# Performance work log

Hardware: AMD Instinct MI355X
Metric: run time of the kernel (lower is better)

Reference implementation:

```python
import jax, jax.numpy as jnp
import numpy as np

B, S, D, H = 2, 2048, 1024, 16
DK = D // H


def setup_inputs() -> dict:
    key = jax.random.key(0)
    ks = jax.random.split(key, 9)
    w_scale = 0.02  # small init for linear weights
    return {
        "query": jax.random.normal(ks[0], (B, S, D), jnp.float32),
        "key": jax.random.normal(ks[1], (B, S, D), jnp.float32),
        "value": jax.random.normal(ks[2], (B, S, D), jnp.float32),
        "mask": jax.random.randint(ks[3], (B, 1, S, S), 0, 2).astype(bool),
        "Wq": jax.random.normal(ks[4], (D, D), jnp.float32) * w_scale,
        "bq": jnp.zeros((D,), jnp.float32),
        "Wk": jax.random.normal(ks[5], (D, D), jnp.float32) * w_scale,
        "bk": jnp.zeros((D,), jnp.float32),
        "Wv": jax.random.normal(ks[6], (D, D), jnp.float32) * w_scale,
        "bv": jnp.zeros((D,), jnp.float32),
        "Wo": jax.random.normal(ks[7], (D, D), jnp.float32) * w_scale,
        "bo": jnp.zeros((D,), jnp.float32),
    }


def _split_heads(x):
    # [B,S,D] -> [B,H,S,DK]
    return x.reshape(B, S, H, DK).transpose(0, 2, 1, 3)


def reference(query, key, value, mask, Wq, bq, Wk, bk, Wv, bv, Wo, bo):
    Q = _split_heads(query @ Wq + bq)
    K = _split_heads(key @ Wk + bk)
    V = _split_heads(value @ Wv + bv)
    scores = jnp.einsum("bhqd,bhkd->bhqk", Q, K) / jnp.sqrt(jnp.float32(DK))
    scores = jnp.where(mask, -jnp.inf, scores)  # masked_fill(mask, -inf)
    attn_w = jax.nn.softmax(scores, axis=-1)
    attn_w = jnp.nan_to_num(attn_w, nan=0.0)  # rows fully masked -> 0
    out = jnp.einsum("bhqk,bhkd->bhqd", attn_w, V)
    out = out.transpose(0, 2, 1, 3).reshape(B, S, D)
    return out @ Wo + bo
```

## Files before the change

kernel.cpp:

```cpp
#include <hip/hip_runtime.h>
#include <hip/hip_bf16.h>
#include <cmath>
#include <cstdint>
#include <cstddef>

#define B_  2
#define S_  2048
#define D_  1024
#define H_  16
#define DK_ 64
#define NEG_BIG (-1e30f)

typedef __attribute__((ext_vector_type(8))) short bf16x8;
typedef __attribute__((ext_vector_type(4))) float f32x4;
typedef __attribute__((ext_vector_type(16))) float f32x16;

static __device__ __forceinline__ unsigned short f2bf(float f) {
  __hip_bfloat16 h = __float2bfloat16(f);
  return *reinterpret_cast<unsigned short*>(&h);
}

static __device__ __forceinline__ unsigned cvtpk(float lo, float hi) {
  unsigned d;
  asm("v_cvt_pk_bf16_f32 %0, %1, %2" : "=v"(d) : "v"(lo), "v"(hi));
  return d;
}
#define SWAP32(a, b) asm("v_permlane32_swap_b32 %0, %1" : "+v"(a), "+v"(b))

__global__ void pack_mask_kernel(const int* __restrict__ mask,
                                 unsigned* __restrict__ bits, int nwords) {
  int i = blockIdx.x * blockDim.x + threadIdx.x;
  if (i >= nwords) return;
  const int* p = mask + (size_t)i * 32;
  unsigned w = 0;
#pragma unroll
  for (int j = 0; j < 32; ++j) w |= (p[j] != 0 ? (1u << j) : 0u);
  bits[i] = w;
}

__global__ void cvt_f32_bf16_kernel(const float* __restrict__ in,
                                    unsigned short* __restrict__ out, int n8) {
  int i = blockIdx.x * blockDim.x + threadIdx.x;
  if (i >= n8) return;
  const float4* p = reinterpret_cast<const float4*>(in) + (size_t)i * 2;
  float4 a = p[0], b = p[1];
  ushort4 o0 = {f2bf(a.x), f2bf(a.y), f2bf(a.z), f2bf(a.w)};
  ushort4 o1 = {f2bf(b.x), f2bf(b.y), f2bf(b.z), f2bf(b.w)};
  ushort4* q = reinterpret_cast<ushort4*>(out) + (size_t)i * 2;
  q[0] = o0;
  q[1] = o1;
}

__global__ __launch_bounds__(256) void transpose_w_kernel(
    const float* __restrict__ W, unsigned short* __restrict__ Wt) {
  __shared__ unsigned short tile[32][33];
  const int r0 = blockIdx.y * 32, c0 = blockIdx.x * 32;
  const int t = threadIdx.x;
  {
    const int r = t >> 3, c4 = (t & 7) * 4;
    float4 v = *reinterpret_cast<const float4*>(&W[(size_t)(r0 + r) * D_ + c0 + c4]);
    tile[c4 + 0][r] = f2bf(v.x);
    tile[c4 + 1][r] = f2bf(v.y);
    tile[c4 + 2][r] = f2bf(v.z);
    tile[c4 + 3][r] = f2bf(v.w);
  }
  __syncthreads();
  {
    const int n = t >> 3, k4 = (t & 7) * 4;
    ushort4 o = {tile[n][k4 + 0], tile[n][k4 + 1], tile[n][k4 + 2], tile[n][k4 + 3]};
    *reinterpret_cast<ushort4*>(&Wt[(size_t)(c0 + n) * D_ + r0 + k4]) = o;
  }
}

template <int MODE>
__global__ __launch_bounds__(256) void gemm_bf16_kernel(
    const unsigned short* __restrict__ A, const unsigned short* __restrict__ Wt,
    const float* __restrict__ bias, void* __restrict__ Cout) {
  constexpr int K = D_;
  __shared__ __attribute__((aligned(16))) unsigned short as_[64 * 32];
  __shared__ __attribute__((aligned(16))) unsigned short bs_[64 * 32];
  const int bm = blockIdx.x * 64, bn = blockIdx.y * 64;
  const int t = threadIdx.x, wv = t >> 6, lane = t & 63;
  const int r = lane & 15, g = lane >> 4;
  const int wm = (wv >> 1) * 32, wn = (wv & 1) * 32;
  const int grow = 16 * wv + (lane >> 2);
  const int gcol = (lane & 3) * 8;

  typedef __attribute__((address_space(3))) unsigned int lds_u32;
  typedef __attribute__((address_space(1))) const unsigned int glb_u32;
  lds_u32* asl = (lds_u32*)(as_ + 16 * wv * 32);
  lds_u32* bsl = (lds_u32*)(bs_ + 16 * wv * 32);

  f32x4 acc[2][2] = {};

  for (int k0 = 0; k0 < K; k0 += 32) {
    __syncthreads();
    __builtin_amdgcn_global_load_lds(
        (glb_u32*)&A[(size_t)(bm + grow) * K + k0 + gcol], asl, 16, 0, 0);
    __builtin_amdgcn_global_load_lds(
        (glb_u32*)&Wt[(size_t)(bn + grow) * K + k0 + gcol], bsl, 16, 0, 0);
    __syncthreads();

    bf16x8 a0 = *reinterpret_cast<const bf16x8*>(&as_[(wm + r) * 32 + 8 * g]);
    bf16x8 a1 = *reinterpret_cast<const bf16x8*>(&as_[(wm + 16 + r) * 32 + 8 * g]);
    bf16x8 b0 = *reinterpret_cast<const bf16x8*>(&bs_[(wn + r) * 32 + 8 * g]);
    bf16x8 b1 = *reinterpret_cast<const bf16x8*>(&bs_[(wn + 16 + r) * 32 + 8 * g]);
    acc[0][0] = __builtin_amdgcn_mfma_f32_16x16x32_bf16(a0, b0, acc[0][0], 0, 0, 0);
    acc[0][1] = __builtin_amdgcn_mfma_f32_16x16x32_bf16(a0, b1, acc[0][1], 0, 0, 0);
    acc[1][0] = __builtin_amdgcn_mfma_f32_16x16x32_bf16(a1, b0, acc[1][0], 0, 0, 0);
    acc[1][1] = __builtin_amdgcn_mfma_f32_16x16x32_bf16(a1, b1, acc[1][1], 0, 0, 0);
  }

#pragma unroll
  for (int mf = 0; mf < 2; ++mf)
#pragma unroll
    for (int nf = 0; nf < 2; ++nf)
#pragma unroll
      for (int reg = 0; reg < 4; ++reg) {
        const int row = bm + wm + 16 * mf + 4 * g + reg;
        const int col = bn + wn + 16 * nf + r;
        float v = acc[mf][nf][reg] + bias[col];
        if constexpr (MODE == 3) {
          ((float*)Cout)[(size_t)row * D_ + col] = v;
        } else {
          const int bb = row >> 11, s = row & (S_ - 1);
          const int h = col >> 6, dk = col & (DK_ - 1);
          unsigned short* o = (unsigned short*)Cout;
          if constexpr (MODE == 0)
            o[(((size_t)(bb * H_ + h)) * S_ + s) * DK_ + dk] = f2bf(v * 0.125f);
          else if constexpr (MODE == 1)
            o[(((size_t)(bb * H_ + h)) * S_ + s) * DK_ + dk] = f2bf(v);
          else
            o[(((size_t)(bb * H_ + h)) * DK_ + dk) * S_ + s] = f2bf(v);
        }
      }
}

__global__ __launch_bounds__(256) void attn_mfma_kernel(
    const unsigned short* __restrict__ Qh, const unsigned short* __restrict__ Kh,
    const unsigned short* __restrict__ VT, const unsigned* __restrict__ mbits,
    unsigned short* __restrict__ ctx) {
  __shared__ float mlds[2][2][32];
  __shared__ float llds[2][2][32];
  __shared__ float olds[2][2][16][64];

  const int flat = blockIdx.x;
  const int bh = (flat & 7) * 4 + ((flat >> 3) & 3);
  const int qblk = flat >> 5;
  const int b = bh >> 4, h = bh & 15;
  const int wv = threadIdx.x >> 6, lane = threadIdx.x & 63;
  const int qsub = wv & 1, khalf = wv >> 1;
  const int ql = lane & 31, hi = lane >> 5;
  const int qrow = qblk * 64 + qsub * 32 + ql;

  const unsigned short* Qrow = &Qh[((size_t)bh * S_ + qrow) * DK_];
  bf16x8 qf[4];
#pragma unroll
  for (int i = 0; i < 4; ++i)
    qf[i] = *(const bf16x8*)&Qrow[16 * i + 8 * hi];

  const unsigned short* Khead = &Kh[(size_t)bh * S_ * DK_];
  const unsigned short* Vhead = &VT[(size_t)bh * DK_ * S_];
  const unsigned* mrow = &mbits[((size_t)b * S_ + qrow) * (S_ / 32)];

  f32x16 o0 = {}, o1 = {};
  float m = NEG_BIG, l = 0.f;

  const int tbeg = khalf * 32, tend = tbeg + 32;
  bf16x8 kf[4];
#pragma unroll
  for (int i = 0; i < 4; ++i)
    kf[i] = *(const bf16x8*)&Khead[(size_t)(tbeg * 32 + ql) * DK_ + 16 * i + 8 * hi];
  unsigned mw = mrow[tbeg];

  for (int tt = tbeg; tt < tend; ++tt) {
    f32x16 sc = {};
#pragma unroll
    for (int i = 0; i < 4; ++i)
      sc = __builtin_amdgcn_mfma_f32_32x32x16_bf16(kf[i], qf[i], sc, 0, 0, 0);

    const int tn = (tt + 1 < tend) ? tt + 1 : tt;
    bf16x8 kn[4];
#pragma unroll
    for (int i = 0; i < 4; ++i)
      kn[i] = *(const bf16x8*)&Khead[(size_t)(tn * 32 + ql) * DK_ + 16 * i + 8 * hi];
    const unsigned mwn = mrow[tn];

    bf16x8 vf[2][2];
#pragma unroll
    for (int kk = 0; kk < 2; ++kk)
#pragma unroll
      for (int db = 0; db < 2; ++db)
        vf[kk][db] = *(const bf16x8*)
            &Vhead[(size_t)(db * 32 + ql) * S_ + tt * 32 + kk * 16 + 8 * hi];

    const unsigned msh = mw >> (4 * hi);
#pragma unroll
    for (int reg = 0; reg < 16; ++reg) {
      const int creg = (reg & 3) + 8 * (reg >> 2);
      if ((msh >> creg) & 1u) sc[reg] = NEG_BIG;
    }

    float px = sc[0];
#pragma unroll
    for (int reg = 1; reg < 16; ++reg) px = fmaxf(px, sc[reg]);
    px = fmaxf(px, __shfl_xor(px, 32));

    if (!__all(px - m <= 8.f)) {
      const float mn = fmaxf(m, px);
      const float alpha = __expf(m - mn);
      m = mn;
      l *= alpha;
#pragma unroll
      for (int reg = 0; reg < 16; ++reg) { o0[reg] *= alpha; o1[reg] *= alpha; }
    }

    float rs = 0.f;
#pragma unroll
    for (int reg = 0; reg < 16; ++reg) {
      sc[reg] = __expf(sc[reg] - m);
      rs += sc[reg];
    }
    rs += __shfl_xor(rs, 32);
    l += rs;

    unsigned w0 = cvtpk(sc[0], sc[1]),   w2p = cvtpk(sc[4], sc[5]);
    unsigned w1 = cvtpk(sc[2], sc[3]),   w3p = cvtpk(sc[6], sc[7]);
    unsigned u0 = cvtpk(sc[8], sc[9]),   u2p = cvtpk(sc[12], sc[13]);
    unsigned u1 = cvtpk(sc[10], sc[11]), u3p = cvtpk(sc[14], sc[15]);
    SWAP32(w0, w2p);
    SWAP32(w1, w3p);
    SWAP32(u0, u2p);
    SWAP32(u1, u3p);
    union { unsigned u[4]; bf16x8 v; } pu0, pu1;
    pu0.u[0] = w0; pu0.u[1] = w1; pu0.u[2] = w2p; pu0.u[3] = w3p;
    pu1.u[0] = u0; pu1.u[1] = u1; pu1.u[2] = u2p; pu1.u[3] = u3p;

    o0 = __builtin_amdgcn_mfma_f32_32x32x16_bf16(pu0.v, vf[0][0], o0, 0, 0, 0);
    o0 = __builtin_amdgcn_mfma_f32_32x32x16_bf16(pu1.v, vf[1][0], o0, 0, 0, 0);
    o1 = __builtin_amdgcn_mfma_f32_32x32x16_bf16(pu0.v, vf[0][1], o1, 0, 0, 0);
    o1 = __builtin_amdgcn_mfma_f32_32x32x16_bf16(pu1.v, vf[1][1], o1, 0, 0, 0);

#pragma unroll
    for (int i = 0; i < 4; ++i) kf[i] = kn[i];
    mw = mwn;
  }

  if (lane < 32) {
    mlds[khalf][qsub][ql] = m;
    llds[khalf][qsub][ql] = l;
  }
  if (khalf == 0) {
#pragma unroll
    for (int reg = 0; reg < 16; ++reg) {
      olds[qsub][0][reg][lane] = o0[reg];
      olds[qsub][1][reg][lane] = o1[reg];
    }
  }
  __syncthreads();
  if (khalf == 1) {
#pragma unroll
    for (int reg = 0; reg < 16; ++reg) {
      const int crow = (reg & 3) + 8 * (reg >> 2) + 4 * hi;
      const float m0 = mlds[0][qsub][crow], l0 = llds[0][qsub][crow];
      const float m1 = mlds[1][qsub][crow], l1 = llds[1][qsub][crow];
      const float ms = fmaxf(m0, m1);
      const float f0 = __expf(m0 - ms), f1 = __expf(m1 - ms);
      const float ls = l0 * f0 + l1 * f1;
      const float inv = (ms == NEG_BIG) ? 0.f : 1.f / ls;
      const float v0 = (olds[qsub][0][reg][lane] * f0 + o0[reg] * f1) * inv;
      const float v1 = (olds[qsub][1][reg][lane] * f0 + o1[reg] * f1) * inv;
      const int q = qblk * 64 + qsub * 32 + crow;
      unsigned short* cp = &ctx[((size_t)(b * S_ + q)) * D_ + h * DK_];
      cp[ql] = f2bf(v0);
      cp[32 + ql] = f2bf(v1);
    }
  }
}

extern "C" void kernel_launch(void* const* d_in, const int* in_sizes, int n_in,
                              void* d_out, int out_size, void* d_ws,
                              size_t ws_size, hipStream_t stream) {
  const float* query = (const float*)d_in[0];
  const float* key   = (const float*)d_in[1];
  const float* value = (const float*)d_in[2];
  const int*   mask  = (const int*)d_in[3];
  const float* Wq = (const float*)d_in[4];
  const float* bq = (const float*)d_in[5];
  const float* Wk = (const float*)d_in[6];
  const float* bk = (const float*)d_in[7];
  const float* Wv = (const float*)d_in[8];
  const float* bv = (const float*)d_in[9];
  const float* Wo = (const float*)d_in[10];
  const float* bo = (const float*)d_in[11];
  float* out = (float*)d_out;

  const size_t nElem = (size_t)B_ * S_ * D_;
  const size_t wElem = (size_t)D_ * D_;
  unsigned short* ws = (unsigned short*)d_ws;
  unsigned short* qb   = ws;
  unsigned short* kb   = qb + nElem;
  unsigned short* vb   = kb + nElem;
  unsigned short* wtq  = vb + nElem;
  unsigned short* wtk  = wtq + wElem;
  unsigned short* wtv  = wtk + wElem;
  unsigned short* wto  = wtv + wElem;
  unsigned short* Qh   = wto + wElem;
  unsigned short* Kh   = Qh + nElem;
  unsigned short* VT   = Kh + nElem;
  unsigned short* ctxb = VT + nElem;
  unsigned* mbits = (unsigned*)(ctxb + nElem);

  {
    const int nwords = B_ * S_ * S_ / 32;
    pack_mask_kernel<<<(nwords + 255) / 256, 256, 0, stream>>>(mask, mbits, nwords);
  }
  {
    const int n8 = (int)(nElem / 8);
    const int blocks = (n8 + 255) / 256;
    cvt_f32_bf16_kernel<<<blocks, 256, 0, stream>>>(query, qb, n8);
    cvt_f32_bf16_kernel<<<blocks, 256, 0, stream>>>(key,   kb, n8);
    cvt_f32_bf16_kernel<<<blocks, 256, 0, stream>>>(value, vb, n8);
  }
  {
    dim3 grid(32, 32);
    transpose_w_kernel<<<grid, 256, 0, stream>>>(Wq, wtq);
    transpose_w_kernel<<<grid, 256, 0, stream>>>(Wk, wtk);
    transpose_w_kernel<<<grid, 256, 0, stream>>>(Wv, wtv);
    transpose_w_kernel<<<grid, 256, 0, stream>>>(Wo, wto);
  }
  {
    dim3 grid(64, 16);
    gemm_bf16_kernel<0><<<grid, 256, 0, stream>>>(qb, wtq, bq, Qh);
    gemm_bf16_kernel<1><<<grid, 256, 0, stream>>>(kb, wtk, bk, Kh);
    gemm_bf16_kernel<2><<<grid, 256, 0, stream>>>(vb, wtv, bv, VT);
  }
  attn_mfma_kernel<<<1024, 256, 0, stream>>>(Qh, Kh, VT, mbits, ctxb);
  {
    dim3 grid(64, 16);
    gemm_bf16_kernel<3><<<grid, 256, 0, stream>>>(ctxb, wto, bo, out);
  }
}
```

Measured before the change: 373.0 us.

## Batch prep/QKV launches, split attention keys four ways, add MFMA priority

The three conversion kernels, the four weight transposes and the three QKV GEMMs are each merged into a single launch that picks its operands by grid z/y index, which cuts launch count and lets the work overlap. The attention kernel now gives each block 32 query rows with four waves each covering a quarter of the keys, doubling the grid to 2048 blocks and merging four partial softmax states through LDS. s_setprio is raised around the MFMA groups. The four-way split adds LDS traffic for the merge and reloads Q for each block.

```diff
diff --git a/kernel.cpp b/kernel.cpp
--- a/kernel.cpp
+++ b/kernel.cpp
@@ -38,22 +38,34 @@
   bits[i] = w;
 }
 
-__global__ void cvt_f32_bf16_kernel(const float* __restrict__ in,
-                                    unsigned short* __restrict__ out, int n8) {
+__global__ void cvt_f32_bf16_kernel(const float* __restrict__ q,
+                                    const float* __restrict__ k,
+                                    const float* __restrict__ v,
+                                    unsigned short* __restrict__ qo,
+                                    unsigned short* __restrict__ ko,
+                                    unsigned short* __restrict__ vo, int n8) {
   int i = blockIdx.x * blockDim.x + threadIdx.x;
   if (i >= n8) return;
+  const float* in = (blockIdx.y == 0) ? q : (blockIdx.y == 1) ? k : v;
+  unsigned short* out = (blockIdx.y == 0) ? qo : (blockIdx.y == 1) ? ko : vo;
   const float4* p = reinterpret_cast<const float4*>(in) + (size_t)i * 2;
   float4 a = p[0], b = p[1];
   ushort4 o0 = {f2bf(a.x), f2bf(a.y), f2bf(a.z), f2bf(a.w)};
   ushort4 o1 = {f2bf(b.x), f2bf(b.y), f2bf(b.z), f2bf(b.w)};
-  ushort4* q = reinterpret_cast<ushort4*>(out) + (size_t)i * 2;
-  q[0] = o0;
-  q[1] = o1;
+  ushort4* o = reinterpret_cast<ushort4*>(out) + (size_t)i * 2;
+  o[0] = o0;
+  o[1] = o1;
 }
 
 __global__ __launch_bounds__(256) void transpose_w_kernel(
-    const float* __restrict__ W, unsigned short* __restrict__ Wt) {
+    const float* __restrict__ w0, const float* __restrict__ w1,
+    const float* __restrict__ w2, const float* __restrict__ w3,
+    unsigned short* __restrict__ t0, unsigned short* __restrict__ t1,
+    unsigned short* __restrict__ t2, unsigned short* __restrict__ t3) {
   __shared__ unsigned short tile[32][33];
+  const int z = blockIdx.z;
+  const float* W = (z == 0) ? w0 : (z == 1) ? w1 : (z == 2) ? w2 : w3;
+  unsigned short* Wt = (z == 0) ? t0 : (z == 1) ? t1 : (z == 2) ? t2 : t3;
   const int r0 = blockIdx.y * 32, c0 = blockIdx.x * 32;
   const int t = threadIdx.x;
   {
@@ -72,10 +84,77 @@
   }
 }
 
-template <int MODE>
-__global__ __launch_bounds__(256) void gemm_bf16_kernel(
+typedef __attribute__((address_space(3))) unsigned int lds_u32;
+typedef __attribute__((address_space(1))) const unsigned int glb_u32;
+
+__global__ __launch_bounds__(256) void qkv_gemm_kernel(
+    const unsigned short* __restrict__ qb, const unsigned short* __restrict__ kb,
+    const unsigned short* __restrict__ vb, const unsigned short* __restrict__ wtq,
+    const unsigned short* __restrict__ wtk, const unsigned short* __restrict__ wtv,
+    const float* __restrict__ bq, const float* __restrict__ bk,
+    const float* __restrict__ bv, unsigned short* __restrict__ Qh,
+    unsigned short* __restrict__ Kh, unsigned short* __restrict__ VT) {
+  constexpr int K = D_;
+  __shared__ __attribute__((aligned(16))) unsigned short as_[64 * 32];
+  __shared__ __attribute__((aligned(16))) unsigned short bs_[64 * 32];
+  const int z = blockIdx.z;
+  const unsigned short* A = (z == 0) ? qb : (z == 1) ? kb : vb;
+  const unsigned short* Wt = (z == 0) ? wtq : (z == 1) ? wtk : wtv;
+  const float* bias = (z == 0) ? bq : (z == 1) ? bk : bv;
+
+  const int bm = blockIdx.x * 64, bn = blockIdx.y * 64;
+  const int t = threadIdx.x, wv = t >> 6, lane = t & 63;
+  const int r = lane & 15, g = lane >> 4;
+  const int wm = (wv >> 1) * 32, wn = (wv & 1) * 32;
+  const int grow = 16 * wv + (lane >> 2);
+  const int gcol = (lane & 3) * 8;
+
+  lds_u32* asl = (lds_u32*)(as_ + 16 * wv * 32);
+  lds_u32* bsl = (lds_u32*)(bs_ + 16 * wv * 32);
+
+  f32x4 acc[2][2] = {};
+
+  for (int k0 = 0; k0 < K; k0 += 32) {
+    __syncthreads();
+    __builtin_amdgcn_global_load_lds(
+        (glb_u32*)&A[(size_t)(bm + grow) * K + k0 + gcol], asl, 16, 0, 0);
+    __builtin_amdgcn_global_load_lds(
+        (glb_u32*)&Wt[(size_t)(bn + grow) * K + k0 + gcol], bsl, 16, 0, 0);
+    __syncthreads();
+
+    bf16x8 a0 = *reinterpret_cast<const bf16x8*>(&as_[(wm + r) * 32 + 8 * g]);
+    bf16x8 a1 = *reinterpret_cast<const bf16x8*>(&as_[(wm + 16 + r) * 32 + 8 * g]);
+    bf16x8 b0 = *reinterpret_cast<const bf16x8*>(&bs_[(wn + r) * 32 + 8 * g]);
+    bf16x8 b1 = *reinterpret_cast<const bf16x8*>(&bs_[(wn + 16 + r) * 32 + 8 * g]);
+    acc[0][0] = __builtin_amdgcn_mfma_f32_16x16x32_bf16(a0, b0, acc[0][0], 0, 0, 0);
+    acc[0][1] = __builtin_amdgcn_mfma_f32_16x16x32_bf16(a0, b1, acc[0][1], 0, 0, 0);
+    acc[1][0] = __builtin_amdgcn_mfma_f32_16x16x32_bf16(a1, b0, acc[1][0], 0, 0, 0);
+    acc[1][1] = __builtin_amdgcn_mfma_f32_16x16x32_bf16(a1, b1, acc[1][1], 0, 0, 0);
+  }
+
+#pragma unroll
+  for (int mf = 0; mf < 2; ++mf)
+#pragma unroll
+    for (int nf = 0; nf < 2; ++nf)
+#pragma unroll
+      for (int reg = 0; reg < 4; ++reg) {
+        const int row = bm + wm + 16 * mf + 4 * g + reg;
+        const int col = bn + wn + 16 * nf + r;
+        const float v = acc[mf][nf][reg] + bias[col];
+        const int bb = row >> 11, s = row & (S_ - 1);
+        const int h = col >> 6, dk = col & (DK_ - 1);
+        if (z == 0)
+          Qh[(((size_t)(bb * H_ + h)) * S_ + s) * DK_ + dk] = f2bf(v * 0.125f);
+        else if (z == 1)
+          Kh[(((size_t)(bb * H_ + h)) * S_ + s) * DK_ + dk] = f2bf(v);
+        else
+          VT[(((size_t)(bb * H_ + h)) * DK_ + dk) * S_ + s] = f2bf(v);
+      }
+}
+
+__global__ __launch_bounds__(256) void out_gemm_kernel(
     const unsigned short* __restrict__ A, const unsigned short* __restrict__ Wt,
-    const float* __restrict__ bias, void* __restrict__ Cout) {
+    const float* __restrict__ bias, float* __restrict__ Cout) {
   constexpr int K = D_;
   __shared__ __attribute__((aligned(16))) unsigned short as_[64 * 32];
   __shared__ __attribute__((aligned(16))) unsigned short bs_[64 * 32];
@@ -86,8 +165,6 @@
   const int grow = 16 * wv + (lane >> 2);
   const int gcol = (lane & 3) * 8;
 
-  typedef __attribute__((address_space(3))) unsigned int lds_u32;
-  typedef __attribute__((address_space(1))) const unsigned int glb_u32;
   lds_u32* asl = (lds_u32*)(as_ + 16 * wv * 32);
   lds_u32* bsl = (lds_u32*)(bs_ + 16 * wv * 32);
 
@@ -119,20 +196,7 @@
       for (int reg = 0; reg < 4; ++reg) {
         const int row = bm + wm + 16 * mf + 4 * g + reg;
         const int col = bn + wn + 16 * nf + r;
-        float v = acc[mf][nf][reg] + bias[col];
-        if constexpr (MODE == 3) {
-          ((float*)Cout)[(size_t)row * D_ + col] = v;
-        } else {
-          const int bb = row >> 11, s = row & (S_ - 1);
-          const int h = col >> 6, dk = col & (DK_ - 1);
-          unsigned short* o = (unsigned short*)Cout;
-          if constexpr (MODE == 0)
-            o[(((size_t)(bb * H_ + h)) * S_ + s) * DK_ + dk] = f2bf(v * 0.125f);
-          else if constexpr (MODE == 1)
-            o[(((size_t)(bb * H_ + h)) * S_ + s) * DK_ + dk] = f2bf(v);
-          else
-            o[(((size_t)(bb * H_ + h)) * DK_ + dk) * S_ + s] = f2bf(v);
-        }
+        Cout[(size_t)row * D_ + col] = acc[mf][nf][reg] + bias[col];
       }
 }
 
@@ -140,18 +204,17 @@
     const unsigned short* __restrict__ Qh, const unsigned short* __restrict__ Kh,
     const unsigned short* __restrict__ VT, const unsigned* __restrict__ mbits,
     unsigned short* __restrict__ ctx) {
-  __shared__ float mlds[2][2][32];
-  __shared__ float llds[2][2][32];
-  __shared__ float olds[2][2][16][64];
+  __shared__ float mlds[4][32];
+  __shared__ float llds[4][32];
+  __shared__ float olds[3][2][16][64];
 
   const int flat = blockIdx.x;
   const int bh = (flat & 7) * 4 + ((flat >> 3) & 3);
   const int qblk = flat >> 5;
   const int b = bh >> 4, h = bh & 15;
-  const int wv = threadIdx.x >> 6, lane = threadIdx.x & 63;
-  const int qsub = wv & 1, khalf = wv >> 1;
+  const int kh = threadIdx.x >> 6, lane = threadIdx.x & 63;
   const int ql = lane & 31, hi = lane >> 5;
-  const int qrow = qblk * 64 + qsub * 32 + ql;
+  const int qrow = qblk * 32 + ql;
 
   const unsigned short* Qrow = &Qh[((size_t)bh * S_ + qrow) * DK_];
   bf16x8 qf[4];
@@ -166,7 +229,7 @@
   f32x16 o0 = {}, o1 = {};
   float m = NEG_BIG, l = 0.f;
 
-  const int tbeg = khalf * 32, tend = tbeg + 32;
+  const int tbeg = kh * 16, tend = tbeg + 16;
   bf16x8 kf[4];
 #pragma unroll
   for (int i = 0; i < 4; ++i)
@@ -175,9 +238,11 @@
 
   for (int tt = tbeg; tt < tend; ++tt) {
     f32x16 sc = {};
+    __builtin_amdgcn_s_setprio(1);
 #pragma unroll
     for (int i = 0; i < 4; ++i)
       sc = __builtin_amdgcn_mfma_f32_32x32x16_bf16(kf[i], qf[i], sc, 0, 0, 0);
+    __builtin_amdgcn_s_setprio(0);
 
     const int tn = (tt + 1 < tend) ? tt + 1 : tt;
     bf16x8 kn[4];
@@ -236,10 +301,12 @@
     pu0.u[0] = w0; pu0.u[1] = w1; pu0.u[2] = w2p; pu0.u[3] = w3p;
     pu1.u[0] = u0; pu1.u[1] = u1; pu1.u[2] = u2p; pu1.u[3] = u3p;
 
+    __builtin_amdgcn_s_setprio(1);
     o0 = __builtin_amdgcn_mfma_f32_32x32x16_bf16(pu0.v, vf[0][0], o0, 0, 0, 0);
     o0 = __builtin_amdgcn_mfma_f32_32x32x16_bf16(pu1.v, vf[1][0], o0, 0, 0, 0);
     o1 = __builtin_amdgcn_mfma_f32_32x32x16_bf16(pu0.v, vf[0][1], o1, 0, 0, 0);
     o1 = __builtin_amdgcn_mfma_f32_32x32x16_bf16(pu1.v, vf[1][1], o1, 0, 0, 0);
+    __builtin_amdgcn_s_setprio(0);
 
 #pragma unroll
     for (int i = 0; i < 4; ++i) kf[i] = kn[i];
@@ -247,30 +314,34 @@
   }
 
   if (lane < 32) {
-    mlds[khalf][qsub][ql] = m;
-    llds[khalf][qsub][ql] = l;
-  }
-  if (khalf == 0) {
+    mlds[kh][ql] = m;
+    llds[kh][ql] = l;
+  }
+  if (kh < 3) {
 #pragma unroll
     for (int reg = 0; reg < 16; ++reg) {
-      olds[qsub][0][reg][lane] = o0[reg];
-      olds[qsub][1][reg][lane] = o1[reg];
+      olds[kh][0][reg][lane] = o0[reg];
+      olds[kh][1][reg][lane] = o1[reg];
     }
   }
   __syncthreads();
-  if (khalf == 1) {
+  if (kh == 3) {
 #pragma unroll
     for (int reg = 0; reg < 16; ++reg) {
       const int crow = (reg & 3) + 8 * (reg >> 2) + 4 * hi;
-      const float m0 = mlds[0][qsub][crow], l0 = llds[0][qsub][crow];
-      const float m1 = mlds[1][qsub][crow], l1 = llds[1][qsub][crow];
-      const float ms = fmaxf(m0, m1);
+      const float m0 = mlds[0][crow], m1 = mlds[1][crow];
+      const float m2 = mlds[2][crow], m3 = mlds[3][crow];
+      const float ms = fmaxf(fmaxf(m0, m1), fmaxf(m2, m3));
       const float f0 = __expf(m0 - ms), f1 = __expf(m1 - ms);
-      const float ls = l0 * f0 + l1 * f1;
+      const float f2 = __expf(m2 - ms), f3 = __expf(m3 - ms);
+      const float ls = llds[0][crow] * f0 + llds[1][crow] * f1 +
+                       llds[2][crow] * f2 + llds[3][crow] * f3;
       const float inv = (ms == NEG_BIG) ? 0.f : 1.f / ls;
-      const float v0 = (olds[qsub][0][reg][lane] * f0 + o0[reg] * f1) * inv;
-      const float v1 = (olds[qsub][1][reg][lane] * f0 + o1[reg] * f1) * inv;
-      const int q = qblk * 64 + qsub * 32 + crow;
+      const float v0 = (olds[0][0][reg][lane] * f0 + olds[1][0][reg][lane] * f1 +
+                        olds[2][0][reg][lane] * f2 + o0[reg] * f3) * inv;
+      const float v1 = (olds[0][1][reg][lane] * f0 + olds[1][1][reg][lane] * f1 +
+                        olds[2][1][reg][lane] * f2 + o1[reg] * f3) * inv;
+      const int q = qblk * 32 + crow;
       unsigned short* cp = &ctx[((size_t)(b * S_ + q)) * D_ + h * DK_];
       cp[ql] = f2bf(v0);
       cp[32 + ql] = f2bf(v1);
@@ -317,27 +388,21 @@
   }
   {
     const int n8 = (int)(nElem / 8);
-    const int blocks = (n8 + 255) / 256;
-    cvt_f32_bf16_kernel<<<blocks, 256, 0, stream>>>(query, qb, n8);
-    cvt_f32_bf16_kernel<<<blocks, 256, 0, stream>>>(key,   kb, n8);
-    cvt_f32_bf16_kernel<<<blocks, 256, 0, stream>>>(value, vb, n8);
-  }
-  {
-    dim3 grid(32, 32);
-    transpose_w_kernel<<<grid, 256, 0, stream>>>(Wq, wtq);
-    transpose_w_kernel<<<grid, 256, 0, stream>>>(Wk, wtk);
-    transpose_w_kernel<<<grid, 256, 0, stream>>>(Wv, wtv);
-    transpose_w_kernel<<<grid, 256, 0, stream>>>(Wo, wto);
-  }
+    dim3 grid((n8 + 255) / 256, 3);
+    cvt_f32_bf16_kernel<<<grid, 256, 0, stream>>>(query, key, value, qb, kb, vb, n8);
+  }
+  {
+    dim3 grid(32, 32, 4);
+    transpose_w_kernel<<<grid, 256, 0, stream>>>(Wq, Wk, Wv, Wo, wtq, wtk, wtv, wto);
+  }
+  {
+    dim3 grid(64, 16, 3);
+    qkv_gemm_kernel<<<grid, 256, 0, stream>>>(qb, kb, vb, wtq, wtk, wtv,
+                                              bq, bk, bv, Qh, Kh, VT);
+  }
+  attn_mfma_kernel<<<2048, 256, 0, stream>>>(Qh, Kh, VT, mbits, ctxb);
   {
     dim3 grid(64, 16);
-    gemm_bf16_kernel<0><<<grid, 256, 0, stream>>>(qb, wtq, bq, Qh);
-    gemm_bf16_kernel<1><<<grid, 256, 0, stream>>>(kb, wtk, bk, Kh);
-    gemm_bf16_kernel<2><<<grid, 256, 0, stream>>>(vb, wtv, bv, VT);
-  }
-  attn_mfma_kernel<<<1024, 256, 0, stream>>>(Qh, Kh, VT, mbits, ctxb);
-  {
-    dim3 grid(64, 16);
-    gemm_bf16_kernel<3><<<grid, 256, 0, stream>>>(ctxb, wto, bo, out);
-  }
-}
+    out_gemm_kernel<<<grid, 256, 0, stream>>>(ctxb, wto, bo, out);
+  }
+}
```

Result: faster. 360.4 us (-3.4%).
